# Kernel tuning notes

Hardware: AMD Instinct MI355X
Metric: run time of the kernel (lower is better)

Reference implementation:

```python
import jax, jax.numpy as jnp
import numpy as np

S, B, I, H = 2048, 64, 128, 128
E = float(np.e)


def setup_inputs() -> dict:
    key = jax.random.key(0)
    ks = jax.random.split(key, 16)
    s = 1.0 / np.sqrt(H)
    inp = {
        "x": jax.random.normal(ks[0], (S, B, I), jnp.float32),
        "h0": jnp.zeros((2, B, H), jnp.float32),
        "c0": jnp.zeros((2, B, H), jnp.float32),
        # elapsed times, strictly positive
        "delta_ts": jax.random.uniform(ks[1], (B, S), jnp.float32, 0.1, 10.0),
    }
    names = ["W_ih", "W_hh", "b_ih", "b_hh", "W_d", "b_d"]
    shapes = [(4 * H, I), (4 * H, H), (4 * H,), (4 * H,), (H, H), (H,)]
    idx = 2
    for d in ["f", "r"]:
        for n, sh in zip(names, shapes):
            inp[f"{n}_{d}"] = jax.random.uniform(ks[idx], sh, jnp.float32, -s, s)
            idx += 1
    return inp


def _run_dir(x, dt, h, c, W_ih, W_hh, b_ih, b_hh, W_d, b_d):
    """Scan a TLSTM cell over time. x: [S,B,I], dt: [S,B]."""
    def step(carry, inp):
        h, c = carry
        xt, dtt = inp
        # time-aware memory decomposition (Baytas et al.)
        c_s = jnp.tanh(c @ W_d.T + b_d)               # short-term memory
        c_adj = c - c_s + c_s / jnp.log(E + dtt[:, None])  # discounted by elapsed time
        gates = xt @ W_ih.T + b_ih + h @ W_hh.T + b_hh
        i_g, f_g, g_g, o_g = jnp.split(gates, 4, axis=-1)
        c_n = jax.nn.sigmoid(f_g) * c_adj + jax.nn.sigmoid(i_g) * jnp.tanh(g_g)
        h_n = jax.nn.sigmoid(o_g) * jnp.tanh(c_n)
        return (h_n, c_n), h_n

    (h, c), ys = jax.lax.scan(step, (h, c), (x, dt))
    return ys, h, c


def reference(x, h0, c0, delta_ts,
              W_ih_f, W_hh_f, b_ih_f, b_hh_f, W_d_f, b_d_f,
              W_ih_r, W_hh_r, b_ih_r, b_hh_r, W_d_r, b_d_r):
    dt = delta_ts.T  # [S, B]
    out_f, _, _ = _run_dir(x, dt, h0[0], c0[0],
                           W_ih_f, W_hh_f, b_ih_f, b_hh_f, W_d_f, b_d_f)
    out_r, _, _ = _run_dir(x[::-1], dt[::-1], h0[1], c0[1],
                           W_ih_r, W_hh_r, b_ih_r, b_hh_r, W_d_r, b_d_r)
    return jnp.concatenate([out_f, out_r[::-1]], axis=-1)  # [S, B, 2H]
```

## Files before the change

### kernel.cpp

```cpp
#include <hip/hip_runtime.h>
#include <hip/hip_bf16.h>

#define SEQ  2048
#define BAT  64
#define HID  128
#define LDSP 136

#define XB_OFF  (1u << 20)
#define IL_OFF  (35u << 20)

typedef __bf16 bf16x8 __attribute__((ext_vector_type(8)));
typedef float  f32x4  __attribute__((ext_vector_type(4)));

#define MFMA(a,b,c) __builtin_amdgcn_mfma_f32_16x16x32_bf16((a),(b),(c),0,0,0)

__device__ __forceinline__ float sig_f(float x) {
    return __fdividef(1.0f, 1.0f + __expf(-x));
}
__device__ __forceinline__ float tanh_f(float x) {
    return 1.0f - __fdividef(2.0f, 1.0f + __expf(2.0f * x));
}
__device__ __forceinline__ bf16x8 cvt8(const float* p) {
    bf16x8 r;
    #pragma unroll
    for (int i = 0; i < 8; ++i) r[i] = (__bf16)p[i];
    return r;
}

__global__ void cvt_x_kernel(const float* __restrict__ x, __bf16* __restrict__ xb) {
    const int i = (blockIdx.x * 256 + threadIdx.x) * 4;
    const float4 v = *reinterpret_cast<const float4*>(x + i);
    __bf16 o[4];
    o[0] = (__bf16)v.x; o[1] = (__bf16)v.y; o[2] = (__bf16)v.z; o[3] = (__bf16)v.w;
    *reinterpret_cast<uint2*>(xb + i) = *reinterpret_cast<const uint2*>(o);
}

__global__ void prep_ilog_kernel(const float* __restrict__ dts, float* __restrict__ il) {
    const int idx = blockIdx.x * 256 + threadIdx.x;
    const int b = idx >> 11, t = idx & 2047;
    const float l = __logf(2.718281828459045f + dts[idx]);
    il[t * BAT + b] = __fdividef(1.0f, l) - 1.0f;
}

__global__ __launch_bounds__(512, 2) void tlstm_main(
    const __bf16* __restrict__ xb,   const float* __restrict__ ilg,
    const float* __restrict__ h0,    const float* __restrict__ c0,
    const float* __restrict__ Wih_f, const float* __restrict__ Whh_f,
    const float* __restrict__ bih_f, const float* __restrict__ bhh_f,
    const float* __restrict__ Wd_f,  const float* __restrict__ bd_f,
    const float* __restrict__ Wih_r, const float* __restrict__ Whh_r,
    const float* __restrict__ bih_r, const float* __restrict__ bhh_r,
    const float* __restrict__ Wd_r,  const float* __restrict__ bd_r,
    float* __restrict__ out)
{
    const int d    = blockIdx.x >> 4;
    const int b0   = (blockIdx.x & 15) * 4;
    const int tid  = threadIdx.x;
    const int w    = tid >> 6;
    const int lane = tid & 63;
    const int nl   = lane & 15;
    const int q    = lane >> 4;
    const int j    = w * 16 + nl;

    const float* Wih = d ? Wih_r : Wih_f;
    const float* Whh = d ? Whh_r : Whh_f;
    const float* bih = d ? bih_r : bih_f;
    const float* bhh = d ? bhh_r : bhh_f;
    const float* Wd  = d ? Wd_r  : Wd_f;
    const float* bd  = d ? bd_r  : bd_f;

    __shared__ __align__(16) __bf16 hc_a[2][16][LDSP];

    bf16x8 whh_fr[4][4], wih_fr[4][4], wd_fr[4];
    #pragma unroll
    for (int g = 0; g < 4; ++g) {
        const int row = g * 128 + j;
        #pragma unroll
        for (int kt = 0; kt < 4; ++kt) {
            const int off = row * HID + kt * 32 + q * 8;
            wih_fr[g][kt] = cvt8(Wih + off);
            whh_fr[g][kt] = cvt8(Whh + off);
        }
    }
    #pragma unroll
    for (int kt = 0; kt < 4; ++kt)
        wd_fr[kt] = cvt8(Wd + j * HID + kt * 32 + q * 8);

    f32x4 bgv[4];
    #pragma unroll
    for (int g = 0; g < 4; ++g) {
        const float b = bih[g * 128 + j] + bhh[g * 128 + j];
        bgv[g] = f32x4{b, b, b, b};
    }
    const float bias_d = bd[j];
    const f32x4 bdv = f32x4{bias_d, bias_d, bias_d, bias_d};

    for (int e = tid; e < 4 * HID; e += 512) {
        const int ci = e >> 7, k = e & 127;
        hc_a[0][ci * 4][k]     = (__bf16)h0[(d * BAT + b0 + ci) * HID + k];
        hc_a[0][ci * 4 + 2][k] = (__bf16)c0[(d * BAT + b0 + ci) * HID + k];
    }
    float c_st = c0[(d * BAT + b0 + q) * HID + j];
    __syncthreads();

    const int t0      = d ? (SEQ - 1) : 0;
    const int tstep   = d ? -1 : 1;
    const int xstride = tstep * BAT * HID;
    const int istride = tstep * BAT;
    const int ostride = tstep * BAT * 256;

    const __bf16* xp0 = xb + (size_t)((t0 + tstep * (nl & 3)) * BAT + b0 + (nl >> 2)) * HID + q * 8;
    const float*  ip0 = ilg + (size_t)t0 * BAT + b0 + q;
    float*        op  = out + (size_t)(t0 * BAT + b0 + q) * 256 + d * 128 + j;

    bf16x8 xfrA[4], xfrB[4];
    float  ilA[4], ilB[4];

    #pragma unroll
    for (int kt = 0; kt < 4; ++kt) {
        xfrA[kt] = *reinterpret_cast<const bf16x8*>(xp0 + kt * 32);
        xfrB[kt] = *reinterpret_cast<const bf16x8*>(xp0 + 4 * xstride + kt * 32);
    }
    #pragma unroll
    for (int dtv = 0; dtv < 4; ++dtv) {
        ilA[dtv] = ip0[dtv * istride];
        ilB[dtv] = ip0[(4 + dtv) * istride];
    }
    const __bf16* xpl = xp0 + 8 * xstride;
    const float*  ipl = ip0 + 8 * istride;

    auto chunk = [&](bf16x8 (&xfrCur)[4], float (&ilCur)[4]) __attribute__((always_inline)) {
        f32x4 x0 = MFMA(xfrCur[0], wih_fr[0][0], bgv[0]);
        f32x4 x1 = MFMA(xfrCur[0], wih_fr[1][0], bgv[1]);
        f32x4 x2 = MFMA(xfrCur[0], wih_fr[2][0], bgv[2]);
        f32x4 x3 = MFMA(xfrCur[0], wih_fr[3][0], bgv[3]);
        #pragma unroll
        for (int kt = 1; kt < 4; ++kt) {
            x0 = MFMA(xfrCur[kt], wih_fr[0][kt], x0);
            x1 = MFMA(xfrCur[kt], wih_fr[1][kt], x1);
            x2 = MFMA(xfrCur[kt], wih_fr[2][kt], x2);
            x3 = MFMA(xfrCur[kt], wih_fr[3][kt], x3);
        }

        #pragma unroll
        for (int dt = 0; dt < 4; ++dt) {
            const int p  = dt & 1;
            const int pn = p ^ 1;
            const int hr = dt;
            const int cr = (dt + 2) & 3;

            const float il_use = ilCur[dt];

            bf16x8 hcfr[4];
            #pragma unroll
            for (int kt = 0; kt < 4; ++kt)
                hcfr[kt] = *reinterpret_cast<const bf16x8*>(&hc_a[p][nl][kt * 32 + q * 8]);

            f32x4 cA = MFMA(hcfr[0], wd_fr[0],     bdv);
            f32x4 g0 = MFMA(hcfr[0], whh_fr[0][0], x0);
            f32x4 g1 = MFMA(hcfr[0], whh_fr[1][0], x1);
            f32x4 g2 = MFMA(hcfr[0], whh_fr[2][0], x2);
            f32x4 g3 = MFMA(hcfr[0], whh_fr[3][0], x3);
            #pragma unroll
            for (int kt = 1; kt < 4; ++kt) {
                cA = MFMA(hcfr[kt], wd_fr[kt],      cA);
                g0 = MFMA(hcfr[kt], whh_fr[0][kt],  g0);
                g1 = MFMA(hcfr[kt], whh_fr[1][kt],  g1);
                g2 = MFMA(hcfr[kt], whh_fr[2][kt],  g2);
                g3 = MFMA(hcfr[kt], whh_fr[3][kt],  g3);
            }

            xfrCur[dt] = *reinterpret_cast<const bf16x8*>(xpl + dt * 32);
            ilCur[dt]  = ipl[dt * istride];

            {
                const float cs   = tanh_f(cA[cr]);
                const float cadj = fmaf(cs, il_use, c_st);
                const float gf   = sig_f(g1[hr]);
                const float gi   = sig_f(g0[hr]);
                const float gg   = tanh_f(g2[hr]);
                const float cn   = gf * cadj + gi * gg;
                hc_a[pn][q * 4 + ((dt + 3) & 3)][j] = (__bf16)cn;
                const float go   = sig_f(g3[hr]);
                const float hn   = go * tanh_f(cn);
                c_st = cn;
                hc_a[pn][q * 4 + ((dt + 1) & 3)][j] = (__bf16)hn;
                *op = hn;
            }
            op += ostride;

            asm volatile("s_waitcnt lgkmcnt(0)\n\ts_barrier" ::: "memory");
        }
        xpl += 4 * xstride;
        ipl += 4 * istride;
    };

    for (int tc = 0; tc < SEQ / 4; tc += 2) {
        chunk(xfrA, ilA);
        chunk(xfrB, ilB);
    }
}

extern "C" void kernel_launch(void* const* d_in, const int* in_sizes, int n_in,
                              void* d_out, int out_size, void* d_ws, size_t ws_size,
                              hipStream_t stream) {
    const float* x     = (const float*)d_in[0];
    const float* h0    = (const float*)d_in[1];
    const float* c0    = (const float*)d_in[2];
    const float* dts   = (const float*)d_in[3];
    const float* Wih_f = (const float*)d_in[4];
    const float* Whh_f = (const float*)d_in[5];
    const float* bih_f = (const float*)d_in[6];
    const float* bhh_f = (const float*)d_in[7];
    const float* Wd_f  = (const float*)d_in[8];
    const float* bd_f  = (const float*)d_in[9];
    const float* Wih_r = (const float*)d_in[10];
    const float* Whh_r = (const float*)d_in[11];
    const float* bih_r = (const float*)d_in[12];
    const float* bhh_r = (const float*)d_in[13];
    const float* Wd_r  = (const float*)d_in[14];
    const float* bd_r  = (const float*)d_in[15];
    float* out = (float*)d_out;

    __bf16* xbuf = (__bf16*)((char*)d_ws + XB_OFF);
    float*  il   = (float*)((char*)d_ws + IL_OFF);

    cvt_x_kernel<<<16384, 256, 0, stream>>>(x, xbuf);
    prep_ilog_kernel<<<512, 256, 0, stream>>>(dts, il);

    tlstm_main<<<32, 512, 0, stream>>>(xbuf, il, h0, c0,
                                       Wih_f, Whh_f, bih_f, bhh_f, Wd_f, bd_f,
                                       Wih_r, Whh_r, bih_r, bhh_r, Wd_r, bd_r,
                                       out);
}
```

Measured before the change: 1.838 ms.

## Software-pipeline input projection MFMAs across timestep chunks

Computes the W_ih·x projection for the next 4-step chunk one gate at a time, interleaved inside the current chunk's per-step recurrent MFMAs. Previously it ran as a 16-MFMA block at the start of each chunk. The goal is to take the input projection off the serial critical path and spread it across the latency slack of the elementwise tail. The cost is extra accumulator registers (two sets of 4 f32x4) and a deeper prefetch of x fragments, which could raise register pressure under launch_bounds(512,2).

```diff
diff --git a/kernel.cpp b/kernel.cpp
--- a/kernel.cpp
+++ b/kernel.cpp
@@ -113,13 +113,31 @@
     const float*  ip0 = ilg + (size_t)t0 * BAT + b0 + q;
     float*        op  = out + (size_t)(t0 * BAT + b0 + q) * 256 + d * 128 + j;
 
-    bf16x8 xfrA[4], xfrB[4];
+    bf16x8 X0[4], X1[4];
+    f32x4  xaccA[4], xaccB[4];
     float  ilA[4], ilB[4];
 
+    {
+        bf16x8 t[4];
+        #pragma unroll
+        for (int kt = 0; kt < 4; ++kt)
+            t[kt] = *reinterpret_cast<const bf16x8*>(xp0 + kt * 32);
+        xaccA[0] = MFMA(t[0], wih_fr[0][0], bgv[0]);
+        xaccA[1] = MFMA(t[0], wih_fr[1][0], bgv[1]);
+        xaccA[2] = MFMA(t[0], wih_fr[2][0], bgv[2]);
+        xaccA[3] = MFMA(t[0], wih_fr[3][0], bgv[3]);
+        #pragma unroll
+        for (int kt = 1; kt < 4; ++kt) {
+            xaccA[0] = MFMA(t[kt], wih_fr[0][kt], xaccA[0]);
+            xaccA[1] = MFMA(t[kt], wih_fr[1][kt], xaccA[1]);
+            xaccA[2] = MFMA(t[kt], wih_fr[2][kt], xaccA[2]);
+            xaccA[3] = MFMA(t[kt], wih_fr[3][kt], xaccA[3]);
+        }
+    }
     #pragma unroll
     for (int kt = 0; kt < 4; ++kt) {
-        xfrA[kt] = *reinterpret_cast<const bf16x8*>(xp0 + kt * 32);
-        xfrB[kt] = *reinterpret_cast<const bf16x8*>(xp0 + 4 * xstride + kt * 32);
+        X1[kt] = *reinterpret_cast<const bf16x8*>(xp0 + 4 * xstride + kt * 32);
+        X0[kt] = *reinterpret_cast<const bf16x8*>(xp0 + 8 * xstride + kt * 32);
     }
     #pragma unroll
     for (int dtv = 0; dtv < 4; ++dtv) {
@@ -129,19 +147,9 @@
     const __bf16* xpl = xp0 + 8 * xstride;
     const float*  ipl = ip0 + 8 * istride;
 
-    auto chunk = [&](bf16x8 (&xfrCur)[4], float (&ilCur)[4]) __attribute__((always_inline)) {
-        f32x4 x0 = MFMA(xfrCur[0], wih_fr[0][0], bgv[0]);
-        f32x4 x1 = MFMA(xfrCur[0], wih_fr[1][0], bgv[1]);
-        f32x4 x2 = MFMA(xfrCur[0], wih_fr[2][0], bgv[2]);
-        f32x4 x3 = MFMA(xfrCur[0], wih_fr[3][0], bgv[3]);
-        #pragma unroll
-        for (int kt = 1; kt < 4; ++kt) {
-            x0 = MFMA(xfrCur[kt], wih_fr[0][kt], x0);
-            x1 = MFMA(xfrCur[kt], wih_fr[1][kt], x1);
-            x2 = MFMA(xfrCur[kt], wih_fr[2][kt], x2);
-            x3 = MFMA(xfrCur[kt], wih_fr[3][kt], x3);
-        }
-
+    auto chunk = [&](f32x4 (&xu)[4], f32x4 (&xnb)[4],
+                     bf16x8 (&xfS)[4], bf16x8 (&xfL)[4],
+                     float (&ilCur)[4]) __attribute__((always_inline)) {
         #pragma unroll
         for (int dt = 0; dt < 4; ++dt) {
             const int p  = dt & 1;
@@ -156,11 +164,14 @@
             for (int kt = 0; kt < 4; ++kt)
                 hcfr[kt] = *reinterpret_cast<const bf16x8*>(&hc_a[p][nl][kt * 32 + q * 8]);
 
+            xfL[dt]    = *reinterpret_cast<const bf16x8*>(xpl + dt * 32);
+            ilCur[dt]  = ipl[dt * istride];
+
             f32x4 cA = MFMA(hcfr[0], wd_fr[0],     bdv);
-            f32x4 g0 = MFMA(hcfr[0], whh_fr[0][0], x0);
-            f32x4 g1 = MFMA(hcfr[0], whh_fr[1][0], x1);
-            f32x4 g2 = MFMA(hcfr[0], whh_fr[2][0], x2);
-            f32x4 g3 = MFMA(hcfr[0], whh_fr[3][0], x3);
+            f32x4 g0 = MFMA(hcfr[0], whh_fr[0][0], xu[0]);
+            f32x4 g1 = MFMA(hcfr[0], whh_fr[1][0], xu[1]);
+            f32x4 g2 = MFMA(hcfr[0], whh_fr[2][0], xu[2]);
+            f32x4 g3 = MFMA(hcfr[0], whh_fr[3][0], xu[3]);
             #pragma unroll
             for (int kt = 1; kt < 4; ++kt) {
                 cA = MFMA(hcfr[kt], wd_fr[kt],      cA);
@@ -170,8 +181,12 @@
                 g3 = MFMA(hcfr[kt], whh_fr[3][kt],  g3);
             }
 
-            xfrCur[dt] = *reinterpret_cast<const bf16x8*>(xpl + dt * 32);
-            ilCur[dt]  = ipl[dt * istride];
+            {
+                f32x4 xs = MFMA(xfS[0], wih_fr[dt][0], bgv[dt]);
+                xs       = MFMA(xfS[1], wih_fr[dt][1], xs);
+                xs       = MFMA(xfS[2], wih_fr[dt][2], xs);
+                xnb[dt]  = MFMA(xfS[3], wih_fr[dt][3], xs);
+            }
 
             {
                 const float cs   = tanh_f(cA[cr]);
@@ -196,8 +211,8 @@
     };
 
     for (int tc = 0; tc < SEQ / 4; tc += 2) {
-        chunk(xfrA, ilA);
-        chunk(xfrB, ilB);
+        chunk(xaccA, xaccB, X1, X0, ilA);
+        chunk(xaccB, xaccA, X0, X1, ilB);
     }
 }
 
```

Result: slower. 2.216 ms (+20.6%).
